# Optimization experiments

Measured on AMD Instinct MI355X. Metric: run time of the kernel, lower is better.

## Reference

```python
import jax, jax.numpy as jnp
import numpy as np

B, N, D = 4, 2048, 512

def setup_inputs() -> dict:
    key = jax.random.key(0)
    ks = jax.random.split(key, 7)
    s = 1.0 / np.sqrt(D)
    return {
        "x": jax.random.normal(ks[0], (B, N, D), dtype=jnp.float32),
        "Wq": jax.random.uniform(ks[1], (D, D), jnp.float32, -s, s),
        "bq": jax.random.uniform(ks[2], (D,), jnp.float32, -s, s),
        "Wk": jax.random.uniform(ks[3], (D, D), jnp.float32, -s, s),
        "bk": jax.random.uniform(ks[4], (D,), jnp.float32, -s, s),
        "Wv": jax.random.uniform(ks[5], (D, D), jnp.float32, -s, s),
        "bv": jax.random.uniform(ks[6], (D,), jnp.float32, -s, s),
    }

def reference(x, Wq, bq, Wk, bk, Wv, bv):
    # QKV projections (torch Linear: y = x @ W^T + b)
    q = jnp.einsum('bnd,ed->bne', x, Wq) + bq
    k = jnp.einsum('bnd,ed->bne', x, Wk) + bk
    v = jnp.einsum('bnd,ed->bne', x, Wv) + bv
    scale = 1.0 / jnp.sqrt(jnp.asarray(q.shape[-1], q.dtype))
    scores = jnp.einsum('bqd,bkd->bqk', q, k) * scale  # [B,N,N]
    weights = jax.nn.softmax(scores, axis=-1)
    return jnp.einsum('bqk,bkd->bqd', weights, v)
```

## Files before the change

kernel.cpp:

```cpp
#include <hip/hip_runtime.h>
#include <cstdint>
#include <cstddef>

#define SEQ 2048
#define DIM 512

using floatx4 = __attribute__((ext_vector_type(4))) float;
using halfx8  = __attribute__((ext_vector_type(8))) _Float16;

__device__ __forceinline__ ushort f2h(float f) {
    _Float16 h = (_Float16)f;
    return __builtin_bit_cast(unsigned short, h);
}

__global__ void prep_k(const float* __restrict__ x,
                       const float* __restrict__ Wq, const float* __restrict__ Wk,
                       const float* __restrict__ Wv,
                       const float* __restrict__ bq, const float* __restrict__ bk,
                       const float* __restrict__ bv,
                       ushort* __restrict__ xh, ushort* __restrict__ wcat,
                       float* __restrict__ bcat) {
    int i = blockIdx.x * 256 + threadIdx.x;
    if (i < 1048576) {
        float4 v = ((const float4*)x)[i];
        ((ushort4*)xh)[i] = make_ushort4(f2h(v.x), f2h(v.y), f2h(v.z), f2h(v.w));
    } else if (i < 1048576 + 196608) {
        int j = i - 1048576;
        int which = j >> 16;
        const float* w = (which == 0) ? Wq : (which == 1) ? Wk : Wv;
        float4 v = ((const float4*)w)[j & 0xFFFF];
        ((ushort4*)wcat)[j] = make_ushort4(f2h(v.x), f2h(v.y), f2h(v.z), f2h(v.w));
    } else if (i < 1048576 + 196608 + 384) {
        int j = i - 1245184;
        const float* bsrc = (j < 128) ? bq : (j < 256) ? bk : bv;
        ((float4*)bcat)[j] = ((const float4*)bsrc)[j & 127];
    }
}


template<int EPI>
__global__ __launch_bounds__(256, 3)
void gemm_k(const ushort* __restrict__ A, const ushort* __restrict__ B,
            void* __restrict__ Cout, const float* __restrict__ bias,
            float* __restrict__ rowsum, ushort* __restrict__ vt,
            int lda, int ldb, int ldc, int kIters, float alpha,
            long sA, long sB, long sC)
{
    __shared__ __align__(16) ushort smem[2][2][4096];
    __shared__ float rsum[128];
    ushort* Ps = &smem[0][0][0];

    const int tid = threadIdx.x;
    const int bz = blockIdx.z;
    int b, kofs;
    if (EPI == 2) { b = bz & 3; kofs = (bz >> 2) * 512; }
    else          { b = bz; kofs = 0; }
    const ushort* Ab = A + (size_t)b * sA + kofs;
    const ushort* Bb = B + (size_t)b * sB + kofs;

    const int m0 = blockIdx.y * 128;
    const int n0 = blockIdx.x * 128;
    const int lane = tid & 63, wave = tid >> 6;
    const int wm = (wave >> 1) * 64, wn = (wave & 1) * 64;
    const int quad = lane >> 4, l16 = lane & 15;
    const int swz = (l16 >> 1) & 3;

    const int s0 = tid, s1 = tid + 256;
    const int r0 = s0 >> 2, r1 = s1 >> 2;
    const int kc0 = (s0 & 3) ^ ((r0 >> 1) & 3);
    const int kc1 = (s1 & 3) ^ ((r1 >> 1) & 3);
    const ushort* gA0 = Ab + (size_t)(m0 + r0) * lda + kc0 * 8;
    const ushort* gA1 = Ab + (size_t)(m0 + r1) * lda + kc1 * 8;
    const ushort* gB0 = Bb + (size_t)(n0 + r0) * ldb + kc0 * 8;
    const ushort* gB1 = Bb + (size_t)(n0 + r1) * ldb + kc1 * 8;

#define STAGE(kk, bufi) do {                                                              \
    int ko = (kk) * 32;                                                                   \
    __builtin_amdgcn_global_load_lds((const __attribute__((address_space(1))) uint32_t*)(gA0 + ko), \
        (__attribute__((address_space(3))) uint32_t*)(&smem[0][bufi][s0 * 8]), 16, 0, 0); \
    __builtin_amdgcn_global_load_lds((const __attribute__((address_space(1))) uint32_t*)(gA1 + ko), \
        (__attribute__((address_space(3))) uint32_t*)(&smem[0][bufi][s1 * 8]), 16, 0, 0); \
    __builtin_amdgcn_global_load_lds((const __attribute__((address_space(1))) uint32_t*)(gB0 + ko), \
        (__attribute__((address_space(3))) uint32_t*)(&smem[1][bufi][s0 * 8]), 16, 0, 0); \
    __builtin_amdgcn_global_load_lds((const __attribute__((address_space(1))) uint32_t*)(gB1 + ko), \
        (__attribute__((address_space(3))) uint32_t*)(&smem[1][bufi][s1 * 8]), 16, 0, 0); \
} while (0)

    int ofsA[4], ofsB[4];
#pragma unroll
    for (int mi = 0; mi < 4; mi++)
        ofsA[mi] = ((wm + mi * 16 + l16) * 4 + (quad ^ swz)) * 8;
#pragma unroll
    for (int ni = 0; ni < 4; ni++)
        ofsB[ni] = ((wn + ni * 16 + l16) * 4 + (quad ^ swz)) * 8;

    floatx4 acc[4][4];
#pragma unroll
    for (int i = 0; i < 4; i++)
#pragma unroll
        for (int j = 0; j < 4; j++)
            acc[i][j] = (floatx4){0.f, 0.f, 0.f, 0.f};

    if (EPI == 1 && tid < 128) rsum[tid] = 0.f;

    STAGE(0, 0);
    for (int it = 0; it < kIters; ++it) {
        __syncthreads();
        const int buf = it & 1;
        if (it + 1 < kIters) STAGE(it + 1, buf ^ 1);
        halfx8 af[4], bfr[4];
#pragma unroll
        for (int mi = 0; mi < 4; mi++) af[mi] = *(const halfx8*)&smem[0][buf][ofsA[mi]];
#pragma unroll
        for (int ni = 0; ni < 4; ni++) bfr[ni] = *(const halfx8*)&smem[1][buf][ofsB[ni]];
#pragma unroll
        for (int mi = 0; mi < 4; mi++)
#pragma unroll
            for (int ni = 0; ni < 4; ni++)
                acc[mi][ni] = __builtin_amdgcn_mfma_f32_16x16x32_f16(af[mi], bfr[ni], acc[mi][ni], 0, 0, 0);
    }
#undef STAGE

    if constexpr (EPI == 2) {
#pragma unroll
        for (int mi = 0; mi < 4; mi++)
#pragma unroll
            for (int ni = 0; ni < 4; ni++) {
                int col = n0 + wn + ni * 16 + l16;
#pragma unroll
                for (int r = 0; r < 4; r++) {
                    int row = m0 + wm + mi * 16 + quad * 4 + r;
                    ((float*)Cout)[(size_t)bz * sC + (size_t)row * ldc + col] = acc[mi][ni][r];
                }
            }
    } else if (EPI == 0 && n0 >= 1024) {
#pragma unroll
        for (int ni = 0; ni < 4; ni++) {
            int col = n0 + wn + ni * 16 + l16;
            float bv = bias[col];
            int e = col - 1024;
#pragma unroll
            for (int mi = 0; mi < 4; mi++) {
                int row0 = m0 + wm + mi * 16 + quad * 4;
                int bb = row0 >> 11;
                int j = row0 & 2047;
                ushort4 pk = make_ushort4(f2h(acc[mi][ni][0] + bv), f2h(acc[mi][ni][1] + bv),
                                          f2h(acc[mi][ni][2] + bv), f2h(acc[mi][ni][3] + bv));
                *(ushort4*)&vt[((size_t)(bb << 9) + e) * 2048 + j] = pk;
            }
        }
    } else {
        float bvv[4];
        if (EPI == 0) {
#pragma unroll
            for (int ni = 0; ni < 4; ni++) bvv[ni] = bias[n0 + wn + ni * 16 + l16];
        }
        __syncthreads();
#pragma unroll
        for (int mi = 0; mi < 4; mi++)
#pragma unroll
            for (int ni = 0; ni < 4; ni++) {
                int col_l = wn + ni * 16 + l16;
                int c = col_l >> 3, w = col_l & 7;
#pragma unroll
                for (int r = 0; r < 4; r++) {
                    int row_l = wm + mi * 16 + quad * 4 + r;
                    float v = (EPI == 1) ? __expf(acc[mi][ni][r] * alpha)
                                         : acc[mi][ni][r] + bvv[ni];
                    Ps[row_l * 128 + ((c ^ (row_l & 7)) << 3) + w] = f2h(v);
                }
            }
        __syncthreads();
        int rr = tid >> 1, h = tid & 1;
        float s = 0.f;
        size_t base = (EPI == 1) ? (size_t)b * sC : 0;
        ushort* dstrow = (ushort*)Cout + base + (size_t)(m0 + rr) * ldc + n0;
#pragma unroll
        for (int j = 0; j < 8; j++) {
            int c = h * 8 + j;
            halfx8 p = *(const halfx8*)&Ps[rr * 128 + ((c ^ (rr & 7)) << 3)];
            if (EPI == 1) {
#pragma unroll
                for (int e = 0; e < 8; e++) s += (float)p[e];
            }
            *(halfx8*)(dstrow + c * 8) = p;
        }
        if (EPI == 1) {
            atomicAdd(&rsum[rr], s);
            __syncthreads();
            if (tid < 128) atomicAdd(&rowsum[b * SEQ + m0 + tid], rsum[tid]);
        }
    }
}

__global__ void reduce_scale_k(const float* __restrict__ part, const float* __restrict__ rowsum,
                               float* __restrict__ out) {
    int i = blockIdx.x * 256 + threadIdx.x;
    int g = i >> 7;
    int b = g >> 11;
    int local = i - (b << 18);
    float4 a = {0.f, 0.f, 0.f, 0.f};
#pragma unroll
    for (int kc = 0; kc < 4; kc++) {
        const float4* p = (const float4*)part + ((size_t)(kc * 4 + b) << 18);
        float4 v = p[local];
        a.x += v.x; a.y += v.y; a.z += v.z; a.w += v.w;
    }
    float inv = 1.0f / rowsum[g];
    float4 o = {a.x * inv, a.y * inv, a.z * inv, a.w * inv};
    ((float4*)out)[i] = o;
}

extern "C" void kernel_launch(void* const* d_in, const int* in_sizes, int n_in,
                              void* d_out, int out_size, void* d_ws, size_t ws_size,
                              hipStream_t stream) {
    const float* x  = (const float*)d_in[0];
    const float* Wq = (const float*)d_in[1];
    const float* bq = (const float*)d_in[2];
    const float* Wk = (const float*)d_in[3];
    const float* bk = (const float*)d_in[4];
    const float* Wv = (const float*)d_in[5];
    const float* bv = (const float*)d_in[6];
    float* out = (float*)d_out;
    char* ws = (char*)d_ws;

    float*  partial = (float*)(ws);
    ushort* xh      = (ushort*)(ws);
    ushort* wcat    = (ushort*)(ws + 8388608);
    float*  bcat    = (float*)(ws + 9961472);
    float*  rowsum  = (float*)(ws + 67108864);
    ushort* Pb      = (ushort*)(ws + 67141632);
    ushort* vt      = (ushort*)(ws + 100696064);
    ushort* qkh     = (ushort*)(ws + 109084672);

    hipMemsetAsync(rowsum, 0, 8192 * 4, stream);
    prep_k<<<4866, 256, 0, stream>>>(x, Wq, Wk, Wv, bq, bk, bv, xh, wcat, bcat);

    gemm_k<0><<<dim3(12, 64, 1), 256, 0, stream>>>(
        xh, wcat, qkh, bcat, nullptr, vt, 512, 512, 1024, 16, 1.0f, 0, 0, 0);

    const float scale = 0.04419417382415922f;
    gemm_k<1><<<dim3(16, 16, 4), 256, 0, stream>>>(
        qkh, qkh + 512, Pb, nullptr, rowsum, nullptr, 1024, 1024, 2048, 16, scale,
        (long)SEQ * 1024, (long)SEQ * 1024, (long)SEQ * SEQ);

    gemm_k<2><<<dim3(4, 16, 16), 256, 0, stream>>>(
        Pb, vt, partial, nullptr, nullptr, nullptr, 2048, 2048, 512, 16, 1.0f,
        (long)SEQ * SEQ, (long)DIM * SEQ, (long)SEQ * DIM);

    reduce_scale_k<<<4096, 256, 0, stream>>>(partial, rowsum, out);
}
```

Before: 190.1 us.

## Normalize PV partials in GEMM epilogue, store fp16 partials, fold rowsum memset into prep

The split-K PV GEMM now multiplies its partial sums by the reciprocal row sum and writes them as fp16 through the swizzled shared-memory epilogue, where before it wrote fp32 partials with scattered stores. The final reduce kernel just adds the four fp16 partials. This halves the partial traffic and coalesces the stores. The rowsum memset moves into the prep kernel to save a launch, and the launch bounds are raised to 4 waves per SIMD to allow more occupancy. Rounding the partials to fp16 adds precision loss, and the tighter register budget may cause spills.

```diff
diff --git a/kernel.cpp b/kernel.cpp
--- a/kernel.cpp
+++ b/kernel.cpp
@@ -19,7 +19,7 @@
                        const float* __restrict__ bq, const float* __restrict__ bk,
                        const float* __restrict__ bv,
                        ushort* __restrict__ xh, ushort* __restrict__ wcat,
-                       float* __restrict__ bcat) {
+                       float* __restrict__ bcat, float* __restrict__ rowsum) {
     int i = blockIdx.x * 256 + threadIdx.x;
     if (i < 1048576) {
         float4 v = ((const float4*)x)[i];
@@ -34,12 +34,15 @@
         int j = i - 1245184;
         const float* bsrc = (j < 128) ? bq : (j < 256) ? bk : bv;
         ((float4*)bcat)[j] = ((const float4*)bsrc)[j & 127];
+    } else if (i < 1048576 + 196608 + 384 + 2048) {
+        int j = i - 1245568;
+        ((float4*)rowsum)[j] = (float4){0.f, 0.f, 0.f, 0.f};
     }
 }
 
 
 template<int EPI>
-__global__ __launch_bounds__(256, 3)
+__global__ __launch_bounds__(256, 4)
 void gemm_k(const ushort* __restrict__ A, const ushort* __restrict__ B,
             void* __restrict__ Cout, const float* __restrict__ bias,
             float* __restrict__ rowsum, ushort* __restrict__ vt,
@@ -121,19 +124,7 @@
     }
 #undef STAGE
 
-    if constexpr (EPI == 2) {
-#pragma unroll
-        for (int mi = 0; mi < 4; mi++)
-#pragma unroll
-            for (int ni = 0; ni < 4; ni++) {
-                int col = n0 + wn + ni * 16 + l16;
-#pragma unroll
-                for (int r = 0; r < 4; r++) {
-                    int row = m0 + wm + mi * 16 + quad * 4 + r;
-                    ((float*)Cout)[(size_t)bz * sC + (size_t)row * ldc + col] = acc[mi][ni][r];
-                }
-            }
-    } else if (EPI == 0 && n0 >= 1024) {
+    if (EPI == 0 && n0 >= 1024) {
 #pragma unroll
         for (int ni = 0; ni < 4; ni++) {
             int col = n0 + wn + ni * 16 + l16;
@@ -155,6 +146,15 @@
 #pragma unroll
             for (int ni = 0; ni < 4; ni++) bvv[ni] = bias[n0 + wn + ni * 16 + l16];
         }
+        float inv[4][4];
+        if (EPI == 2) {
+#pragma unroll
+            for (int mi = 0; mi < 4; mi++)
+#pragma unroll
+                for (int r = 0; r < 4; r++)
+                    inv[mi][r] = __builtin_amdgcn_rcpf(
+                        rowsum[b * SEQ + m0 + wm + mi * 16 + quad * 4 + r]);
+        }
         __syncthreads();
 #pragma unroll
         for (int mi = 0; mi < 4; mi++)
@@ -166,6 +166,7 @@
                 for (int r = 0; r < 4; r++) {
                     int row_l = wm + mi * 16 + quad * 4 + r;
                     float v = (EPI == 1) ? __expf(acc[mi][ni][r] * alpha)
+                            : (EPI == 2) ? acc[mi][ni][r] * inv[mi][r]
                                          : acc[mi][ni][r] + bvv[ni];
                     Ps[row_l * 128 + ((c ^ (row_l & 7)) << 3) + w] = f2h(v);
                 }
@@ -173,7 +174,7 @@
         __syncthreads();
         int rr = tid >> 1, h = tid & 1;
         float s = 0.f;
-        size_t base = (EPI == 1) ? (size_t)b * sC : 0;
+        size_t base = (EPI == 1) ? (size_t)b * sC : (EPI == 2) ? (size_t)bz * sC : 0;
         ushort* dstrow = (ushort*)Cout + base + (size_t)(m0 + rr) * ldc + n0;
 #pragma unroll
         for (int j = 0; j < 8; j++) {
@@ -193,22 +194,22 @@
     }
 }
 
-__global__ void reduce_scale_k(const float* __restrict__ part, const float* __restrict__ rowsum,
-                               float* __restrict__ out) {
-    int i = blockIdx.x * 256 + threadIdx.x;
-    int g = i >> 7;
-    int b = g >> 11;
-    int local = i - (b << 18);
-    float4 a = {0.f, 0.f, 0.f, 0.f};
+__global__ void reduce_k(const ushort* __restrict__ part, float* __restrict__ out) {
+    int t = blockIdx.x * 256 + threadIdx.x;
+    size_t E = (size_t)t * 8;
+    int b = (int)(E >> 20);
+    size_t le = E & ((1u << 20) - 1);
+    float acc[8] = {0,0,0,0,0,0,0,0};
 #pragma unroll
     for (int kc = 0; kc < 4; kc++) {
-        const float4* p = (const float4*)part + ((size_t)(kc * 4 + b) << 18);
-        float4 v = p[local];
-        a.x += v.x; a.y += v.y; a.z += v.z; a.w += v.w;
-    }
-    float inv = 1.0f / rowsum[g];
-    float4 o = {a.x * inv, a.y * inv, a.z * inv, a.w * inv};
-    ((float4*)out)[i] = o;
+        halfx8 p = *(const halfx8*)&part[(((size_t)(kc * 4 + b)) << 20) + le];
+#pragma unroll
+        for (int e = 0; e < 8; e++) acc[e] += (float)p[e];
+    }
+    float4 o0 = {acc[0], acc[1], acc[2], acc[3]};
+    float4 o1 = {acc[4], acc[5], acc[6], acc[7]};
+    ((float4*)(out + E))[0] = o0;
+    ((float4*)(out + E))[1] = o1;
 }
 
 extern "C" void kernel_launch(void* const* d_in, const int* in_sizes, int n_in,
@@ -224,17 +225,16 @@
     float* out = (float*)d_out;
     char* ws = (char*)d_ws;
 
-    float*  partial = (float*)(ws);
+    ushort* partial = (ushort*)(ws);
     ushort* xh      = (ushort*)(ws);
     ushort* wcat    = (ushort*)(ws + 8388608);
     float*  bcat    = (float*)(ws + 9961472);
-    float*  rowsum  = (float*)(ws + 67108864);
-    ushort* Pb      = (ushort*)(ws + 67141632);
-    ushort* vt      = (ushort*)(ws + 100696064);
-    ushort* qkh     = (ushort*)(ws + 109084672);
-
-    hipMemsetAsync(rowsum, 0, 8192 * 4, stream);
-    prep_k<<<4866, 256, 0, stream>>>(x, Wq, Wk, Wv, bq, bk, bv, xh, wcat, bcat);
+    float*  rowsum  = (float*)(ws + 33554432);
+    ushort* Pb      = (ushort*)(ws + 33587200);
+    ushort* vt      = (ushort*)(ws + 67141632);
+    ushort* qkh     = (ushort*)(ws + 75530240);
+
+    prep_k<<<4874, 256, 0, stream>>>(x, Wq, Wk, Wv, bq, bk, bv, xh, wcat, bcat, rowsum);
 
     gemm_k<0><<<dim3(12, 64, 1), 256, 0, stream>>>(
         xh, wcat, qkh, bcat, nullptr, vt, 512, 512, 1024, 16, 1.0f, 0, 0, 0);
@@ -245,8 +245,8 @@
         (long)SEQ * 1024, (long)SEQ * 1024, (long)SEQ * SEQ);
 
     gemm_k<2><<<dim3(4, 16, 16), 256, 0, stream>>>(
-        Pb, vt, partial, nullptr, nullptr, nullptr, 2048, 2048, 512, 16, 1.0f,
+        Pb, vt, partial, nullptr, rowsum, nullptr, 2048, 2048, 512, 16, 1.0f,
         (long)SEQ * SEQ, (long)DIM * SEQ, (long)SEQ * DIM);
 
-    reduce_scale_k<<<4096, 256, 0, stream>>>(partial, rowsum, out);
-}
+    reduce_k<<<2048, 256, 0, stream>>>(partial, out);
+}
```

Result: faster. 185.9 us (-2.2%).
